# Performance work log

Measured on AMD Instinct MI355X. Metric: run time of the kernel, lower is better.

The kernel has to match this reference:

```python
import jax, jax.numpy as jnp
import numpy as np

B, N, F, C = 1024, 60, 1024, 2


def setup_inputs() -> dict:
    key = jax.random.key(0)
    k1, k2, k3, k4, k5, k6 = jax.random.split(key, 6)
    return {
        "x1": jax.random.normal(k1, (B, N, F), dtype=jnp.float32),
        "x2": jax.random.normal(k2, (B, N, F), dtype=jnp.float32),
        "fc_w": jax.random.normal(k3, (C, F), dtype=jnp.float32) * 0.02,
        "fc_b": jax.random.normal(k4, (C,), dtype=jnp.float32) * 0.02,
        "q_w": jax.random.normal(k5, (F, F), dtype=jnp.float32) * 0.02,
        "q_b": jax.random.normal(k6, (F,), dtype=jnp.float32) * 0.02,
    }


def reference(x1, x2, fc_w, fc_b, q_w, q_b):
    # select_class_max: per-class argmax over instances, then gather the
    # corresponding instance feature rows (sort descending + m_indices[0,:]
    # == argmax along the instance dim).  Dropout p=0.0 is identity.
    def top1_select(x):
        logits = x @ fc_w.T + fc_b              # [B, N, C]
        idx = jnp.argmax(logits, axis=1)        # [B, C]
        return jnp.take_along_axis(x, idx[:, :, None], axis=1)  # [B, C, F]

    h1 = top1_select(x1)
    h2 = top1_select(x2)

    L = jnp.concatenate((x1, x2), axis=1)       # [B, 2N, F]
    n = x1.shape[1]                              # 60 (hardcoded in original)
    scale = 1.0 / jnp.sqrt(jnp.float32(L.shape[2]))

    def q_net(h):
        return jnp.tanh(h) @ q_w.T + q_b        # [B, C, F]

    def attend(h):
        qm = q_net(h)                            # [B, C, F]
        A = jax.nn.softmax(jnp.einsum('bnf,bcf->bnc', L, qm) * scale, axis=1)
        out = 0.9 * jnp.einsum('bnc,bnf->bcf', A, L) + 0.1 * qm  # [B, C, F]
        return A, out

    A1, o1 = attend(h1)
    A2, o2 = attend(h2)

    ATT1 = A1[:, :n, :1]
    ATT2 = A2[:, n:, :1]
    att11 = A1[:, :n, 1:].sum(axis=2)
    att22 = A2[:, n:, 1:].sum(axis=2)
    att12 = A1[:, n:, 1:].sum(axis=2)
    att21 = A2[:, :n, 1:].sum(axis=2)

    x = jnp.concatenate((o1, o2), axis=2)        # [B, C, 2F]
    return (x, o1, o2, h1, h2, ATT1, ATT2, att11, att22, att12, att21)
```

## Files before the change

### kernel.cpp

```cpp
#include <hip/hip_runtime.h>
#include <hip/hip_bf16.h>
#include <hip/hip_fp16.h>

#define BB 1024
#define NN 60
#define FF 1024
#define NT 120

#define OFF_X    0u
#define OFF_O1   4194304u
#define OFF_O2   6291456u
#define OFF_H1   8388608u
#define OFF_H2   10485760u
#define OFF_ATT1 12582912u
#define OFF_ATT2 12644352u
#define OFF_A11  12705792u
#define OFF_A22  12767232u
#define OFF_A12  12828672u
#define OFF_A21  12890112u

typedef float f32x4 __attribute__((ext_vector_type(4)));
typedef _Float16 f16x8 __attribute__((ext_vector_type(8)));

__global__ __launch_bounds__(256) void k_select(const float* __restrict__ x1,
                                                const float* __restrict__ x2,
                                                const float* __restrict__ fc_w,
                                                float* __restrict__ out) {
  const int ba = blockIdx.x;
  const int b = ba >> 1, a = ba & 1;
  const float* xb = (a ? x2 : x1) + (size_t)b * NN * FF;
  const int tid = threadIdx.x, lane = tid & 63, wid = tid >> 6;

  __shared__ float lg[NN][2];
  __shared__ int idx_s[2];

  float w0[16], w1[16];
#pragma unroll
  for (int t = 0; t < 16; ++t) {
    w0[t] = fc_w[t * 64 + lane];
    w1[t] = fc_w[FF + t * 64 + lane];
  }

  for (int i = 0; i < 15; ++i) {
    const int n = wid * 15 + i;
    const float* rp = xb + (size_t)n * FF;
    float a0 = 0.f, a1 = 0.f;
#pragma unroll
    for (int t = 0; t < 16; ++t) {
      const float v = rp[t * 64 + lane];
      a0 += v * w0[t];
      a1 += v * w1[t];
    }
    for (int off = 32; off; off >>= 1) {
      a0 += __shfl_xor(a0, off);
      a1 += __shfl_xor(a1, off);
    }
    if (lane == 0) { lg[n][0] = a0; lg[n][1] = a1; }
  }
  __syncthreads();

  if (wid == 0) {
    for (int c = 0; c < 2; ++c) {
      float v = (lane < NN) ? lg[lane][c] : -3e38f;
      int idx = lane;
      for (int off = 32; off; off >>= 1) {
        const float ov = __shfl_xor(v, off);
        const int oi = __shfl_xor(idx, off);
        if (ov > v || (ov == v && oi < idx)) { v = ov; idx = oi; }
      }
      if (lane == 0) idx_s[c] = idx;
    }
  }
  __syncthreads();

  float* hout = out + (a ? OFF_H2 : OFF_H1) + (size_t)b * 2 * FF;
  for (int c = 0; c < 2; ++c) {
    const float4* rp4 = (const float4*)(xb + (size_t)idx_s[c] * FF);
    float4* ho4 = (float4*)(hout + c * FF);
    ho4[tid] = rp4[tid];
  }
}

__global__ __launch_bounds__(256) void k_prep(const float* __restrict__ h,
                                              const float* __restrict__ q_w,
                                              _Float16* __restrict__ Tb,
                                              _Float16* __restrict__ Wb) {
  const int T4 = 4096 * 1024 / 4;
  const int W4 = 1024 * 1024 / 4;
  const int stride = gridDim.x * blockDim.x;
  for (int i = blockIdx.x * blockDim.x + threadIdx.x; i < T4 + W4; i += stride) {
    if (i < T4) {
      const float4 v = ((const float4*)h)[i];
      union { _Float16 hh[4]; uint2 u; } pk;
      pk.hh[0] = (_Float16)tanhf(v.x);
      pk.hh[1] = (_Float16)tanhf(v.y);
      pk.hh[2] = (_Float16)tanhf(v.z);
      pk.hh[3] = (_Float16)tanhf(v.w);
      ((uint2*)Tb)[i] = pk.u;
    } else {
      const int j = i - T4;
      const float4 v = ((const float4*)q_w)[j];
      union { _Float16 hh[4]; uint2 u; } pk;
      pk.hh[0] = (_Float16)v.x;
      pk.hh[1] = (_Float16)v.y;
      pk.hh[2] = (_Float16)v.z;
      pk.hh[3] = (_Float16)v.w;
      ((uint2*)Wb)[j] = pk.u;
    }
  }
}

__global__ __launch_bounds__(256) void k_qm(const _Float16* __restrict__ Tb,
                                            const _Float16* __restrict__ Wb,
                                            const float* __restrict__ q_b,
                                            float* __restrict__ Qm) {
  const int m0 = blockIdx.x * 64;
  const int n0 = blockIdx.y * 64;
  const int tid = threadIdx.x, lane = tid & 63, wid = tid >> 6;
  const int wm = wid & 1, wn = wid >> 1;

  __shared__ _Float16 As[64][32];
  __shared__ _Float16 Bs[64][32];

  f32x4 acc[2][2] = {};

  const int lrow = tid >> 2;
  const int lcol = (tid & 3) * 8;
  const int ms = wm * 32 + (lane & 15);
  const int ns = wn * 32 + (lane & 15);
  const int ks = (lane >> 4) * 8;

  for (int k0 = 0; k0 < 1024; k0 += 32) {
    __syncthreads();
    *(uint4*)(&As[lrow][lcol]) = *(const uint4*)(Tb + (size_t)(m0 + lrow) * 1024 + k0 + lcol);
    *(uint4*)(&Bs[lrow][lcol]) = *(const uint4*)(Wb + (size_t)(n0 + lrow) * 1024 + k0 + lcol);
    __syncthreads();
#pragma unroll
    for (int mi = 0; mi < 2; ++mi) {
      const f16x8 af = *(const f16x8*)(&As[ms + mi * 16][ks]);
#pragma unroll
      for (int ni = 0; ni < 2; ++ni) {
        const f16x8 bf = *(const f16x8*)(&Bs[ns + ni * 16][ks]);
        acc[mi][ni] = __builtin_amdgcn_mfma_f32_16x16x32_f16(af, bf, acc[mi][ni], 0, 0, 0);
      }
    }
  }

  const int col = lane & 15, quad = lane >> 4;
#pragma unroll
  for (int mi = 0; mi < 2; ++mi) {
#pragma unroll
    for (int ni = 0; ni < 2; ++ni) {
      const int n = n0 + wn * 32 + ni * 16 + col;
      const float qb = q_b[n];
#pragma unroll
      for (int r = 0; r < 4; ++r) {
        const int m = m0 + wm * 32 + mi * 16 + quad * 4 + r;
        Qm[(size_t)m * 1024 + n] = acc[mi][ni][r] + qb;
      }
    }
  }
}

__global__ __launch_bounds__(256) void k_attend(const float* __restrict__ x1,
                                                const float* __restrict__ x2,
                                                const float* __restrict__ Qm,
                                                float* __restrict__ out) {
  const int b = blockIdx.x;
  const int tid = threadIdx.x, lane = tid & 63, wid = tid >> 6;

  __shared__ float qm_l[4][FF];
  __shared__ float s_l[4][128];

#pragma unroll
  for (int j = 0; j < 4; ++j) {
    const int r = (j >> 1) * 2048 + b * 2 + (j & 1);
    ((float4*)qm_l[j])[tid] = ((const float4*)(Qm + (size_t)r * FF))[tid];
  }
  __syncthreads();

  const float* xb1 = x1 + (size_t)b * NN * FF;
  const float* xb2 = x2 + (size_t)b * NN * FF;

  float qr[4][16];
#pragma unroll
  for (int j = 0; j < 4; ++j)
#pragma unroll
    for (int t = 0; t < 16; ++t) qr[j][t] = qm_l[j][t * 64 + lane];

  for (int i = 0; i < 30; ++i) {
    const int n = wid * 30 + i;
    const float* rp = (n < NN) ? (xb1 + (size_t)n * FF) : (xb2 + (size_t)(n - NN) * FF);
    float a0 = 0.f, a1 = 0.f, a2 = 0.f, a3 = 0.f;
#pragma unroll
    for (int t = 0; t < 16; ++t) {
      const float v = rp[t * 64 + lane];
      a0 += v * qr[0][t];
      a1 += v * qr[1][t];
      a2 += v * qr[2][t];
      a3 += v * qr[3][t];
    }
    for (int off = 32; off; off >>= 1) {
      a0 += __shfl_xor(a0, off);
      a1 += __shfl_xor(a1, off);
      a2 += __shfl_xor(a2, off);
      a3 += __shfl_xor(a3, off);
    }
    if (lane == 0) {
      s_l[0][n] = a0 * 0.03125f;
      s_l[1][n] = a1 * 0.03125f;
      s_l[2][n] = a2 * 0.03125f;
      s_l[3][n] = a3 * 0.03125f;
    }
  }
  __syncthreads();

  {
    const int j = wid;
    const bool has1 = (lane + 64) < NT;
    const float v0 = s_l[j][lane];
    const float v1 = has1 ? s_l[j][lane + 64] : -3e38f;
    float m = fmaxf(v0, v1);
    for (int off = 32; off; off >>= 1) m = fmaxf(m, __shfl_xor(m, off));
    const float e0 = expf(v0 - m);
    const float e1 = has1 ? expf(v1 - m) : 0.f;
    float d = e0 + e1;
    for (int off = 32; off; off >>= 1) d += __shfl_xor(d, off);
    const float inv = 1.f / d;
    const float p0 = e0 * inv, p1 = e1 * inv;
    s_l[j][lane] = p0;
    if (has1) s_l[j][lane + 64] = p1;

    const int nb = b * NN;
    if (j == 0) {
      if (lane < NN) out[OFF_ATT1 + nb + lane] = p0;
    } else if (j == 1) {
      if (lane < NN) out[OFF_A11 + nb + lane] = p0;
      if (lane >= NN) out[OFF_A12 + nb + (lane - NN)] = p0;
      if (has1) out[OFF_A12 + nb + (lane + 4)] = p1;
    } else if (j == 2) {
      if (lane >= NN) out[OFF_ATT2 + nb + (lane - NN)] = p0;
      if (has1) out[OFF_ATT2 + nb + (lane + 4)] = p1;
    } else {
      if (lane >= NN) out[OFF_A22 + nb + (lane - NN)] = p0;
      if (has1) out[OFF_A22 + nb + (lane + 4)] = p1;
      if (lane < NN) out[OFF_A21 + nb + lane] = p0;
    }
  }
  __syncthreads();

  {
    float acc[4][4] = {};
    const int f = tid * 4;
    for (int n = 0; n < NT; ++n) {
      const float* rp = (n < NN) ? (xb1 + (size_t)n * FF) : (xb2 + (size_t)(n - NN) * FF);
      const float4 v = *(const float4*)(rp + f);
      const float ve0 = v.x, ve1 = v.y, ve2 = v.z, ve3 = v.w;
#pragma unroll
      for (int j = 0; j < 4; ++j) {
        const float w = s_l[j][n];
        acc[j][0] += w * ve0;
        acc[j][1] += w * ve1;
        acc[j][2] += w * ve2;
        acc[j][3] += w * ve3;
      }
    }
#pragma unroll
    for (int j = 0; j < 4; ++j) {
      const int aa = j >> 1, c = j & 1;
      float4 r;
      r.x = 0.9f * acc[j][0] + 0.1f * qm_l[j][f + 0];
      r.y = 0.9f * acc[j][1] + 0.1f * qm_l[j][f + 1];
      r.z = 0.9f * acc[j][2] + 0.1f * qm_l[j][f + 2];
      r.w = 0.9f * acc[j][3] + 0.1f * qm_l[j][f + 3];
      float* o = out + (aa ? OFF_O2 : OFF_O1) + ((size_t)b * 2 + c) * FF + f;
      *(float4*)o = r;
      float* xo = out + OFF_X + ((size_t)b * 2 + c) * 2048 + aa * FF + f;
      *(float4*)xo = r;
    }
  }
}

extern "C" void kernel_launch(void* const* d_in, const int* in_sizes, int n_in,
                              void* d_out, int out_size, void* d_ws, size_t ws_size,
                              hipStream_t stream) {
  const float* x1 = (const float*)d_in[0];
  const float* x2 = (const float*)d_in[1];
  const float* fc_w = (const float*)d_in[2];
  const float* q_w = (const float*)d_in[4];
  const float* q_b = (const float*)d_in[5];
  float* out = (float*)d_out;

  _Float16* Tb = (_Float16*)d_ws;
  _Float16* Wb = Tb + 4096 * 1024;
  float* Qm = (float*)(Wb + 1024 * 1024);

  k_select<<<2 * BB, 256, 0, stream>>>(x1, x2, fc_w, out);
  k_prep<<<2048, 256, 0, stream>>>(out + OFF_H1, q_w, Tb, Wb);
  k_qm<<<dim3(64, 16), 256, 0, stream>>>(Tb, Wb, q_b, Qm);
  k_attend<<<BB, 256, 0, stream>>>(x1, x2, Qm, out);
}
```

Baseline: 714.3 us.

## Fuse tanh/fp16 packing into select, enlarge GEMM tiles, vectorize attend loads

The tanh-and-fp16 conversion of the selected rows moves into k_select, so the separate h re-read pass is gone and only q_w still gets its own small conversion kernel. The qm GEMM tile grows from 64x64 to 128x128 with padded shared memory, giving more MFMA work per load. The row loads in k_select and k_attend become float4, attend processes two rows per iteration, and the softmax weights are stored transposed for float4 reads. The larger GEMM tile launches only 256 blocks, which may underfill the GPU, and it raises register use.

```diff
diff --git a/kernel.cpp b/kernel.cpp
--- a/kernel.cpp
+++ b/kernel.cpp
@@ -22,10 +22,15 @@
 typedef float f32x4 __attribute__((ext_vector_type(4)));
 typedef _Float16 f16x8 __attribute__((ext_vector_type(8)));
 
+__device__ __forceinline__ float dot4(const float4 a, const float4 b) {
+  return a.x * b.x + a.y * b.y + a.z * b.z + a.w * b.w;
+}
+
 __global__ __launch_bounds__(256) void k_select(const float* __restrict__ x1,
                                                 const float* __restrict__ x2,
                                                 const float* __restrict__ fc_w,
-                                                float* __restrict__ out) {
+                                                float* __restrict__ out,
+                                                _Float16* __restrict__ Tb) {
   const int ba = blockIdx.x;
   const int b = ba >> 1, a = ba & 1;
   const float* xb = (a ? x2 : x1) + (size_t)b * NN * FF;
@@ -34,22 +39,24 @@
   __shared__ float lg[NN][2];
   __shared__ int idx_s[2];
 
-  float w0[16], w1[16];
-#pragma unroll
-  for (int t = 0; t < 16; ++t) {
-    w0[t] = fc_w[t * 64 + lane];
-    w1[t] = fc_w[FF + t * 64 + lane];
+  float4 w0[4], w1[4];
+#pragma unroll
+  for (int t = 0; t < 4; ++t) {
+    w0[t] = *(const float4*)(fc_w + t * 256 + lane * 4);
+    w1[t] = *(const float4*)(fc_w + FF + t * 256 + lane * 4);
   }
 
   for (int i = 0; i < 15; ++i) {
     const int n = wid * 15 + i;
     const float* rp = xb + (size_t)n * FF;
+    float4 v[4];
+#pragma unroll
+    for (int t = 0; t < 4; ++t) v[t] = *(const float4*)(rp + t * 256 + lane * 4);
     float a0 = 0.f, a1 = 0.f;
 #pragma unroll
-    for (int t = 0; t < 16; ++t) {
-      const float v = rp[t * 64 + lane];
-      a0 += v * w0[t];
-      a1 += v * w1[t];
+    for (int t = 0; t < 4; ++t) {
+      a0 += dot4(v[t], w0[t]);
+      a1 += dot4(v[t], w1[t]);
     }
     for (int off = 32; off; off >>= 1) {
       a0 += __shfl_xor(a0, off);
@@ -74,88 +81,83 @@
   __syncthreads();
 
   float* hout = out + (a ? OFF_H2 : OFF_H1) + (size_t)b * 2 * FF;
+  _Float16* tout = Tb + ((size_t)a * 2048 + (size_t)b * 2) * FF;
   for (int c = 0; c < 2; ++c) {
-    const float4* rp4 = (const float4*)(xb + (size_t)idx_s[c] * FF);
-    float4* ho4 = (float4*)(hout + c * FF);
-    ho4[tid] = rp4[tid];
-  }
-}
-
-__global__ __launch_bounds__(256) void k_prep(const float* __restrict__ h,
-                                              const float* __restrict__ q_w,
-                                              _Float16* __restrict__ Tb,
-                                              _Float16* __restrict__ Wb) {
-  const int T4 = 4096 * 1024 / 4;
-  const int W4 = 1024 * 1024 / 4;
-  const int stride = gridDim.x * blockDim.x;
-  for (int i = blockIdx.x * blockDim.x + threadIdx.x; i < T4 + W4; i += stride) {
-    if (i < T4) {
-      const float4 v = ((const float4*)h)[i];
-      union { _Float16 hh[4]; uint2 u; } pk;
-      pk.hh[0] = (_Float16)tanhf(v.x);
-      pk.hh[1] = (_Float16)tanhf(v.y);
-      pk.hh[2] = (_Float16)tanhf(v.z);
-      pk.hh[3] = (_Float16)tanhf(v.w);
-      ((uint2*)Tb)[i] = pk.u;
-    } else {
-      const int j = i - T4;
-      const float4 v = ((const float4*)q_w)[j];
-      union { _Float16 hh[4]; uint2 u; } pk;
-      pk.hh[0] = (_Float16)v.x;
-      pk.hh[1] = (_Float16)v.y;
-      pk.hh[2] = (_Float16)v.z;
-      pk.hh[3] = (_Float16)v.w;
-      ((uint2*)Wb)[j] = pk.u;
-    }
-  }
+    const float4 v = ((const float4*)(xb + (size_t)idx_s[c] * FF))[tid];
+    ((float4*)(hout + c * FF))[tid] = v;
+    union { _Float16 hh[4]; uint2 u; } pk;
+    pk.hh[0] = (_Float16)tanhf(v.x);
+    pk.hh[1] = (_Float16)tanhf(v.y);
+    pk.hh[2] = (_Float16)tanhf(v.z);
+    pk.hh[3] = (_Float16)tanhf(v.w);
+    ((uint2*)(tout + c * FF))[tid] = pk.u;
+  }
+}
+
+__global__ __launch_bounds__(256) void k_prepw(const float* __restrict__ q_w,
+                                               _Float16* __restrict__ Wb) {
+  const int i = blockIdx.x * 256 + threadIdx.x;
+  const float4 v = ((const float4*)q_w)[i];
+  union { _Float16 hh[4]; uint2 u; } pk;
+  pk.hh[0] = (_Float16)v.x;
+  pk.hh[1] = (_Float16)v.y;
+  pk.hh[2] = (_Float16)v.z;
+  pk.hh[3] = (_Float16)v.w;
+  ((uint2*)Wb)[i] = pk.u;
 }
 
 __global__ __launch_bounds__(256) void k_qm(const _Float16* __restrict__ Tb,
                                             const _Float16* __restrict__ Wb,
                                             const float* __restrict__ q_b,
                                             float* __restrict__ Qm) {
-  const int m0 = blockIdx.x * 64;
-  const int n0 = blockIdx.y * 64;
+  const int m0 = blockIdx.x * 128;
+  const int n0 = blockIdx.y * 128;
   const int tid = threadIdx.x, lane = tid & 63, wid = tid >> 6;
   const int wm = wid & 1, wn = wid >> 1;
 
-  __shared__ _Float16 As[64][32];
-  __shared__ _Float16 Bs[64][32];
-
-  f32x4 acc[2][2] = {};
-
-  const int lrow = tid >> 2;
-  const int lcol = (tid & 3) * 8;
-  const int ms = wm * 32 + (lane & 15);
-  const int ns = wn * 32 + (lane & 15);
+  __shared__ _Float16 As[128][40];
+  __shared__ _Float16 Bs[128][40];
+
+  f32x4 acc[4][4] = {};
+
+  const int srow = tid >> 1;
+  const int scol = (tid & 1) * 16;
+  const int fr = lane & 15;
   const int ks = (lane >> 4) * 8;
+
+  const _Float16* Ag = Tb + (size_t)(m0 + srow) * 1024 + scol;
+  const _Float16* Bg = Wb + (size_t)(n0 + srow) * 1024 + scol;
 
   for (int k0 = 0; k0 < 1024; k0 += 32) {
     __syncthreads();
-    *(uint4*)(&As[lrow][lcol]) = *(const uint4*)(Tb + (size_t)(m0 + lrow) * 1024 + k0 + lcol);
-    *(uint4*)(&Bs[lrow][lcol]) = *(const uint4*)(Wb + (size_t)(n0 + lrow) * 1024 + k0 + lcol);
+    *(uint4*)(&As[srow][scol])     = *(const uint4*)(Ag + k0);
+    *(uint4*)(&As[srow][scol + 8]) = *(const uint4*)(Ag + k0 + 8);
+    *(uint4*)(&Bs[srow][scol])     = *(const uint4*)(Bg + k0);
+    *(uint4*)(&Bs[srow][scol + 8]) = *(const uint4*)(Bg + k0 + 8);
     __syncthreads();
-#pragma unroll
-    for (int mi = 0; mi < 2; ++mi) {
-      const f16x8 af = *(const f16x8*)(&As[ms + mi * 16][ks]);
-#pragma unroll
-      for (int ni = 0; ni < 2; ++ni) {
-        const f16x8 bf = *(const f16x8*)(&Bs[ns + ni * 16][ks]);
-        acc[mi][ni] = __builtin_amdgcn_mfma_f32_16x16x32_f16(af, bf, acc[mi][ni], 0, 0, 0);
-      }
-    }
+
+    f16x8 af[4], bf[4];
+#pragma unroll
+    for (int mi = 0; mi < 4; ++mi) af[mi] = *(const f16x8*)(&As[wm * 64 + mi * 16 + fr][ks]);
+#pragma unroll
+    for (int ni = 0; ni < 4; ++ni) bf[ni] = *(const f16x8*)(&Bs[wn * 64 + ni * 16 + fr][ks]);
+#pragma unroll
+    for (int mi = 0; mi < 4; ++mi)
+#pragma unroll
+      for (int ni = 0; ni < 4; ++ni)
+        acc[mi][ni] = __builtin_amdgcn_mfma_f32_16x16x32_f16(af[mi], bf[ni], acc[mi][ni], 0, 0, 0);
   }
 
   const int col = lane & 15, quad = lane >> 4;
 #pragma unroll
-  for (int mi = 0; mi < 2; ++mi) {
-#pragma unroll
-    for (int ni = 0; ni < 2; ++ni) {
-      const int n = n0 + wn * 32 + ni * 16 + col;
-      const float qb = q_b[n];
+  for (int ni = 0; ni < 4; ++ni) {
+    const int n = n0 + wn * 64 + ni * 16 + col;
+    const float qb = q_b[n];
+#pragma unroll
+    for (int mi = 0; mi < 4; ++mi) {
 #pragma unroll
       for (int r = 0; r < 4; ++r) {
-        const int m = m0 + wm * 32 + mi * 16 + quad * 4 + r;
+        const int m = m0 + wm * 64 + mi * 16 + quad * 4 + r;
         Qm[(size_t)m * 1024 + n] = acc[mi][ni][r] + qb;
       }
     }
@@ -171,6 +173,7 @@
 
   __shared__ float qm_l[4][FF];
   __shared__ float s_l[4][128];
+  __shared__ float s_t[128][4];
 
 #pragma unroll
   for (int j = 0; j < 4; ++j) {
@@ -182,35 +185,44 @@
   const float* xb1 = x1 + (size_t)b * NN * FF;
   const float* xb2 = x2 + (size_t)b * NN * FF;
 
-  float qr[4][16];
+  float4 qr[4][4];
 #pragma unroll
   for (int j = 0; j < 4; ++j)
 #pragma unroll
-    for (int t = 0; t < 16; ++t) qr[j][t] = qm_l[j][t * 64 + lane];
-
-  for (int i = 0; i < 30; ++i) {
-    const int n = wid * 30 + i;
-    const float* rp = (n < NN) ? (xb1 + (size_t)n * FF) : (xb2 + (size_t)(n - NN) * FF);
-    float a0 = 0.f, a1 = 0.f, a2 = 0.f, a3 = 0.f;
-#pragma unroll
-    for (int t = 0; t < 16; ++t) {
-      const float v = rp[t * 64 + lane];
-      a0 += v * qr[0][t];
-      a1 += v * qr[1][t];
-      a2 += v * qr[2][t];
-      a3 += v * qr[3][t];
+    for (int t = 0; t < 4; ++t) qr[j][t] = *(const float4*)(&qm_l[j][t * 256 + lane * 4]);
+
+  for (int i = 0; i < 30; i += 2) {
+    const int n0 = wid * 30 + i, n1 = n0 + 1;
+    const float* rp0 = (n0 < NN) ? (xb1 + (size_t)n0 * FF) : (xb2 + (size_t)(n0 - NN) * FF);
+    const float* rp1 = (n1 < NN) ? (xb1 + (size_t)n1 * FF) : (xb2 + (size_t)(n1 - NN) * FF);
+    float4 u[4], v[4];
+#pragma unroll
+    for (int t = 0; t < 4; ++t) {
+      u[t] = *(const float4*)(rp0 + t * 256 + lane * 4);
+      v[t] = *(const float4*)(rp1 + t * 256 + lane * 4);
+    }
+    float acc0[4] = {0.f, 0.f, 0.f, 0.f}, acc1[4] = {0.f, 0.f, 0.f, 0.f};
+#pragma unroll
+    for (int t = 0; t < 4; ++t) {
+#pragma unroll
+      for (int j = 0; j < 4; ++j) {
+        acc0[j] += dot4(u[t], qr[j][t]);
+        acc1[j] += dot4(v[t], qr[j][t]);
+      }
     }
     for (int off = 32; off; off >>= 1) {
-      a0 += __shfl_xor(a0, off);
-      a1 += __shfl_xor(a1, off);
-      a2 += __shfl_xor(a2, off);
-      a3 += __shfl_xor(a3, off);
+#pragma unroll
+      for (int j = 0; j < 4; ++j) {
+        acc0[j] += __shfl_xor(acc0[j], off);
+        acc1[j] += __shfl_xor(acc1[j], off);
+      }
     }
     if (lane == 0) {
-      s_l[0][n] = a0 * 0.03125f;
-      s_l[1][n] = a1 * 0.03125f;
-      s_l[2][n] = a2 * 0.03125f;
-      s_l[3][n] = a3 * 0.03125f;
+#pragma unroll
+      for (int j = 0; j < 4; ++j) {
+        s_l[j][n0] = acc0[j] * 0.03125f;
+        s_l[j][n1] = acc1[j] * 0.03125f;
+      }
     }
   }
   __syncthreads();
@@ -228,8 +240,8 @@
     for (int off = 32; off; off >>= 1) d += __shfl_xor(d, off);
     const float inv = 1.f / d;
     const float p0 = e0 * inv, p1 = e1 * inv;
-    s_l[j][lane] = p0;
-    if (has1) s_l[j][lane + 64] = p1;
+    s_t[lane][j] = p0;
+    if (has1) s_t[lane + 64][j] = p1;
 
     const int nb = b * NN;
     if (j == 0) {
@@ -252,18 +264,31 @@
   {
     float acc[4][4] = {};
     const int f = tid * 4;
-    for (int n = 0; n < NT; ++n) {
-      const float* rp = (n < NN) ? (xb1 + (size_t)n * FF) : (xb2 + (size_t)(n - NN) * FF);
-      const float4 v = *(const float4*)(rp + f);
-      const float ve0 = v.x, ve1 = v.y, ve2 = v.z, ve3 = v.w;
-#pragma unroll
-      for (int j = 0; j < 4; ++j) {
-        const float w = s_l[j][n];
-        acc[j][0] += w * ve0;
-        acc[j][1] += w * ve1;
-        acc[j][2] += w * ve2;
-        acc[j][3] += w * ve3;
-      }
+    for (int n = 0; n < NT; n += 2) {
+      const float* rp0 = (n < NN) ? (xb1 + (size_t)n * FF) : (xb2 + (size_t)(n - NN) * FF);
+      const float* rp1 = (n + 1 < NN) ? (xb1 + (size_t)(n + 1) * FF) : (xb2 + (size_t)(n + 1 - NN) * FF);
+      const float4 v0 = *(const float4*)(rp0 + f);
+      const float4 v1 = *(const float4*)(rp1 + f);
+      const float4 A0 = *(const float4*)(&s_t[n][0]);
+      const float4 A1 = *(const float4*)(&s_t[n + 1][0]);
+      const float w00 = A0.x, w01 = A0.y, w02 = A0.z, w03 = A0.w;
+      const float w10 = A1.x, w11 = A1.y, w12 = A1.z, w13 = A1.w;
+      acc[0][0] += w00 * v0.x + w10 * v1.x;
+      acc[0][1] += w00 * v0.y + w10 * v1.y;
+      acc[0][2] += w00 * v0.z + w10 * v1.z;
+      acc[0][3] += w00 * v0.w + w10 * v1.w;
+      acc[1][0] += w01 * v0.x + w11 * v1.x;
+      acc[1][1] += w01 * v0.y + w11 * v1.y;
+      acc[1][2] += w01 * v0.z + w11 * v1.z;
+      acc[1][3] += w01 * v0.w + w11 * v1.w;
+      acc[2][0] += w02 * v0.x + w12 * v1.x;
+      acc[2][1] += w02 * v0.y + w12 * v1.y;
+      acc[2][2] += w02 * v0.z + w12 * v1.z;
+      acc[2][3] += w02 * v0.w + w12 * v1.w;
+      acc[3][0] += w03 * v0.x + w13 * v1.x;
+      acc[3][1] += w03 * v0.y + w13 * v1.y;
+      acc[3][2] += w03 * v0.z + w13 * v1.z;
+      acc[3][3] += w03 * v0.w + w13 * v1.w;
     }
 #pragma unroll
     for (int j = 0; j < 4; ++j) {
@@ -295,8 +320,8 @@
   _Float16* Wb = Tb + 4096 * 1024;
   float* Qm = (float*)(Wb + 1024 * 1024);
 
-  k_select<<<2 * BB, 256, 0, stream>>>(x1, x2, fc_w, out);
-  k_prep<<<2048, 256, 0, stream>>>(out + OFF_H1, q_w, Tb, Wb);
-  k_qm<<<dim3(64, 16), 256, 0, stream>>>(Tb, Wb, q_b, Qm);
+  k_select<<<2 * BB, 256, 0, stream>>>(x1, x2, fc_w, out, Tb);
+  k_prepw<<<1024, 256, 0, stream>>>(q_w, Wb);
+  k_qm<<<dim3(32, 8), 256, 0, stream>>>(Tb, Wb, q_b, Qm);
   k_attend<<<BB, 256, 0, stream>>>(x1, x2, Qm, out);
 }
```

Result: no change. 705.3 us (-1.3%).
